# Kernel optimization log

Hardware: AMD Instinct MI355X
Metric: run time of the kernel (lower is better)

Reference implementation:

```python
import jax, jax.numpy as jnp
import numpy as np

V = 4          # number of views (fixed in module)
N = 1536       # number of regions/nodes
D = 256        # embedding_size
TOPK = 32      # top-k sparsification
NHEADS = 4     # MultiheadAttention heads
HD = D // NHEADS


def setup_inputs() -> dict:
    key = jax.random.key(0)
    ks = jax.random.split(key, 10)
    s = 1.0 / np.sqrt(D)
    return {
        "H": jax.random.normal(ks[0], (V, N, D), jnp.float32),
        "C": jax.random.uniform(ks[1], (V, V, N, N), jnp.float32),
        "WQ": jax.random.normal(ks[2], (V, D, D), jnp.float32) * s,
        "WK": jax.random.normal(ks[3], (V, D, D), jnp.float32) * s,
        "WV": jax.random.normal(ks[4], (V, D, D), jnp.float32) * s,
        "in_proj_w": jax.random.normal(ks[5], (3 * D, D), jnp.float32) * s,
        "in_proj_b": jnp.zeros((3 * D,), jnp.float32),
        "out_w": jax.random.normal(ks[6], (D, D), jnp.float32) * s,
        "out_b": jnp.zeros((D,), jnp.float32),
        "alphas": jnp.full((V,), 0.95, jnp.float32),   # [alpha_n, alpha_poi, alpha_s, alpha_d]
        "alpha_align": jnp.asarray(0.5, jnp.float32),
        "beta": jnp.asarray(0.5, jnp.float32),
    }


def reference(H, C, WQ, WK, WV, in_proj_w, in_proj_b, out_w, out_b, alphas, alpha_align, beta):
    # ---------------- IRCVA: MultiheadAttention over seq of 4 views, batch = N ----------------
    # H: (V, N, D); torch MHA (batch_first=False): L=V, batch=N
    qkv = jnp.einsum('lnd,ed->lne', H, in_proj_w) + in_proj_b       # (V, N, 3D)
    q, k, v = jnp.split(qkv, 3, axis=-1)

    def to_heads(x):  # (V, N, D) -> (N, h, V, hd)
        return x.reshape(V, N, NHEADS, HD).transpose(1, 2, 0, 3)

    qh, kh, vh = to_heads(q), to_heads(k), to_heads(v)
    att = jax.nn.softmax(jnp.einsum('nhld,nhmd->nhlm', qh, kh) / np.sqrt(HD), axis=-1)
    o = jnp.einsum('nhlm,nhmd->nhld', att, vh).transpose(2, 0, 1, 3).reshape(V, N, D)
    fusion = jnp.einsum('lnd,ed->lne', o, out_w) + out_b             # (V, N, D)
    a = alphas[:, None, None]
    aligned = fusion * a + (1.0 - a) * H                             # (V, N, D)

    # ---------------- CRCVA: top-k sparsified cross-view attention ----------------
    # per-view linear projections (torch Linear: y = x @ W.T)
    Qn = jnp.einsum('vnd,ved->vne', aligned, WQ)
    Kn = jnp.einsum('vnd,ved->vne', aligned, WK)
    Vn = jnp.einsum('vnd,ved->vne', aligned, WV)

    # row-wise top-k of C, scattered back to dense (V, V, N, N)
    vals, idx = jax.lax.top_k(C, TOPK)                               # (V, V, N, K)
    vi = jnp.arange(V)[:, None, None, None]
    qi = jnp.arange(V)[None, :, None, None]
    ni = jnp.arange(N)[None, None, :, None]
    sparse = jnp.zeros_like(C).at[vi, qi, ni, idx].set(vals)
    sparse = sparse * (1.0 - jnp.eye(V, dtype=C.dtype))[:, :, None, None]  # p==q pairs are zero
    C_hat = sparse / (jnp.sum(sparse, axis=-1, keepdims=True) + 1e-12)

    mask = (C_hat > 0).astype(C.dtype)
    scores = jnp.einsum('pnd,qmd->pqnm', Qn, Kn) / np.sqrt(D)        # (V, V, N, N)
    scores = scores * mask + (1.0 - mask) * (-1e9)
    alpha_nbr = jax.nn.softmax(scores, axis=-1)
    # original sums over ALL q (including q==p, which yields uniform attention -> mean of Vn[q])
    nbr = jnp.einsum('pqnm,qmd->pnd', alpha_nbr, Vn)                 # (V, N, D)

    # ---------------- fuse ----------------
    aa = jax.nn.sigmoid(alpha_align)
    f_fuse = jax.nn.relu(aa * aligned + (1.0 - aa) * nbr)
    b = jax.nn.sigmoid(beta)
    return b * H + (1.0 - b) * f_fuse                                # (V, N, D)
```

## Files before the change

kernel.cpp:

```cpp
#include <hip/hip_runtime.h>
#include <hip/hip_bf16.h>

#define VV 4
#define NN 1536
#define DD 256
#define TOPKN 32

typedef unsigned long long ull;
typedef unsigned int u32;
typedef unsigned short u16;
typedef __attribute__((ext_vector_type(8))) short bf16x8;
typedef __attribute__((ext_vector_type(4))) float f32x4;

__device__ __forceinline__ float us2f(u16 u) {
    return __uint_as_float(((u32)u) << 16);
}

__device__ __forceinline__ float sniff_scalar(const void* p, int idx) {
    const u16* u16p = (const u16*)p;
    float bf0 = us2f(u16p[0]);
    float a = fabsf(bf0);
    if (a > 0.01f && a < 100.0f) return us2f(u16p[idx]);
    return ((const float*)p)[idx];
}

__device__ __forceinline__ float gload(const void* p, size_t i, bool isbf) {
    return isbf ? us2f(((const u16*)p)[i]) : ((const float*)p)[i];
}

__device__ __forceinline__ void split_hl(float x, u16& h, u16& l) {
    u32 b = __float_as_uint(x);
    h = (u16)(b >> 16);
    float hf = __uint_as_float(b & 0xffff0000u);
    l = (u16)(__float_as_uint(x - hf) >> 16);
}

__device__ __forceinline__ int classify_wave(const void* p, int lane) {
    const u16* u = (const u16*)p;
    int z = 0, ins = 0;
    #pragma unroll
    for (int k0 = 0; k0 < 128; k0 += 64) {
        int k = k0 + lane;
        u16 lo = u[2 * k], hi = u[2 * k + 1];
        if (lo == 0) z++;
        if (((lo >> 7) & 0xFF) >= 133) ins++;
        if (((hi >> 7) & 0xFF) >= 133) ins++;
    }
    #pragma unroll
    for (int off = 32; off > 0; off >>= 1) {
        z += __shfl_xor(z, off, 64);
        ins += __shfl_xor(ins, off, 64);
    }
    if (z >= 100) return 0;
    if (ins >= 16) return 0;
    return 1;
}

__global__ __launch_bounds__(512) void sniff_kernel(
    const void* __restrict__ H, const void* __restrict__ C,
    const void* __restrict__ WQ, const void* __restrict__ WK,
    const void* __restrict__ WV, const void* __restrict__ inw,
    const void* __restrict__ outw, int* __restrict__ flags)
{
    int wv = threadIdx.x >> 6, lane = threadIdx.x & 63;
    const void* ps[7] = {H, C, WQ, WK, WV, inw, outw};
    if (wv < 7) {
        int f = classify_wave(ps[wv], lane);
        if (lane == 0) flags[wv] = f;
    }
}

__global__ __launch_bounds__(256) void prep_all(
    const void* __restrict__ H, const void* __restrict__ inw,
    const void* __restrict__ outw, const void* __restrict__ WQ,
    const void* __restrict__ WK, const void* __restrict__ WV,
    u16* __restrict__ Hh, u16* __restrict__ Hl,
    u16* __restrict__ iwh, u16* __restrict__ iwl,
    u16* __restrict__ owh, u16* __restrict__ owl,
    u16* __restrict__ wqh, u16* __restrict__ wql,
    u16* __restrict__ wkh, u16* __restrict__ wkl,
    u16* __restrict__ wvh, u16* __restrict__ wvl,
    const int* __restrict__ flags)
{
    const void* src; u16 *dh, *dl; int cnt, fi;
    switch (blockIdx.y) {
        case 0:  src = H;   dh = Hh;  dl = Hl;  cnt = 6144 * 256; fi = 0; break;
        case 1:  src = inw; dh = iwh; dl = iwl; cnt = 768 * 256;  fi = 5; break;
        case 2:  src = outw;dh = owh; dl = owl; cnt = 256 * 256;  fi = 6; break;
        case 3:  src = WQ;  dh = wqh; dl = wql; cnt = VV*256*256; fi = 2; break;
        case 4:  src = WK;  dh = wkh; dl = wkl; cnt = VV*256*256; fi = 3; break;
        default: src = WV;  dh = wvh; dl = wvl; cnt = VV*256*256; fi = 4; break;
    }
    int i0 = (blockIdx.x * 256 + threadIdx.x) * 4;
    if (i0 >= cnt) return;
    bool isbf = flags[fi] != 0;
    #pragma unroll
    for (int u = 0; u < 4; ++u) {
        float x = gload(src, (size_t)(i0 + u), isbf);
        u16 h, l;
        split_hl(x, h, l);
        dh[i0 + u] = h;
        dl[i0 + u] = l;
    }
}

template <int MODE>
__global__ __launch_bounds__(256) void gemm_mfma(
    const u16* __restrict__ Ah_, const u16* __restrict__ Al_,
    const u16* __restrict__ Bh_, const u16* __restrict__ Bl_,
    const u16* __restrict__ Bh2, const u16* __restrict__ Bl2,
    const u16* __restrict__ Bh3, const u16* __restrict__ Bl3,
    float* __restrict__ out0, float* __restrict__ out1, float* __restrict__ out2,
    u16* __restrict__ oH, u16* __restrict__ oL,
    int M, int E, int K,
    const void* __restrict__ Hin, const void* __restrict__ alphas,
    const int* __restrict__ flags)
{
    __shared__ __align__(16) u16 Ahs[128][40];
    __shared__ __align__(16) u16 Als[128][40];
    __shared__ __align__(16) u16 Bhs[128][40];
    __shared__ __align__(16) u16 Bls[128][40];

    int tid = threadIdx.x;
    int wv = tid >> 6, lane = tid & 63;
    int m0 = blockIdx.x * 128, e0 = blockIdx.y * 128;
    int wr = (wv >> 1) * 64, wc = (wv & 1) * 64;

    const u16* Ah = Ah_;
    const u16* Al = Al_;
    const u16* Bh = Bh_;
    const u16* Bl = Bl_;
    float* outp = out0;
    if (MODE == 2) {
        int v = blockIdx.z / 3, s = blockIdx.z % 3;
        size_t aOff = (size_t)v * (NN * 256);
        size_t bOff = (size_t)v * (256 * 256);
        Ah = Ah_ + aOff; Al = Al_ + aOff;
        Bh = (s == 0 ? Bh_ : s == 1 ? Bh2 : Bh3) + bOff;
        Bl = (s == 0 ? Bl_ : s == 1 ? Bl2 : Bl3) + bOff;
        outp = (s == 0 ? out0 : s == 1 ? out1 : out2) + (size_t)v * (NN * 256);
    }

    f32x4 acc[4][4];
    #pragma unroll
    for (int i = 0; i < 4; ++i)
        #pragma unroll
        for (int j = 0; j < 4; ++j)
            acc[i][j] = (f32x4){0.f, 0.f, 0.f, 0.f};

    int fr = lane & 15;
    int kg = (lane >> 4) << 3;

    for (int k0 = 0; k0 < K; k0 += 32) {
        #pragma unroll
        for (int q = 0; q < 2; ++q) {
            int idx8 = tid + (q << 8);
            int r = idx8 >> 2;
            int kc = (idx8 & 3) << 3;
            size_t ga = (size_t)(m0 + r) * K + k0 + kc;
            size_t gb = (size_t)(e0 + r) * K + k0 + kc;
            *(uint4*)&Ahs[r][kc] = *(const uint4*)(Ah + ga);
            *(uint4*)&Als[r][kc] = *(const uint4*)(Al + ga);
            *(uint4*)&Bhs[r][kc] = *(const uint4*)(Bh + gb);
            *(uint4*)&Bls[r][kc] = *(const uint4*)(Bl + gb);
        }
        __syncthreads();

        bf16x8 fah[4], fal[4], fbh[4], fbl[4];
        #pragma unroll
        for (int i = 0; i < 4; ++i) {
            fah[i] = *(const bf16x8*)&Ahs[wr + (i << 4) + fr][kg];
            fal[i] = *(const bf16x8*)&Als[wr + (i << 4) + fr][kg];
            fbh[i] = *(const bf16x8*)&Bhs[wc + (i << 4) + fr][kg];
            fbl[i] = *(const bf16x8*)&Bls[wc + (i << 4) + fr][kg];
        }
        #pragma unroll
        for (int i = 0; i < 4; ++i)
            #pragma unroll
            for (int j = 0; j < 4; ++j) {
                acc[i][j] = __builtin_amdgcn_mfma_f32_16x16x32_bf16(fah[i], fbh[j], acc[i][j], 0, 0, 0);
                acc[i][j] = __builtin_amdgcn_mfma_f32_16x16x32_bf16(fah[i], fbl[j], acc[i][j], 0, 0, 0);
                acc[i][j] = __builtin_amdgcn_mfma_f32_16x16x32_bf16(fal[i], fbh[j], acc[i][j], 0, 0, 0);
            }
        __syncthreads();
    }

    float a_epi = 0.f;
    bool h_bf = false;
    if (MODE == 1) {
        a_epi = sniff_scalar(alphas, m0 / NN);
        h_bf = flags[0] != 0;
    }
    int col = lane & 15;
    int rb = (lane >> 4) << 2;
    #pragma unroll
    for (int i = 0; i < 4; ++i)
        #pragma unroll
        for (int j = 0; j < 4; ++j)
            #pragma unroll
            for (int rr = 0; rr < 4; ++rr) {
                int m = m0 + wr + (i << 4) + rb + rr;
                int e = e0 + wc + (j << 4) + col;
                float v = acc[i][j][rr];
                size_t oi = (size_t)m * E + e;
                if (MODE == 1) {
                    float h = gload(Hin, oi, h_bf);
                    v = a_epi * v + (1.0f - a_epi) * h;
                    u16 hh, ll;
                    split_hl(v, hh, ll);
                    oH[oi] = hh;
                    oL[oi] = ll;
                }
                outp[oi] = v;
            }
}

__global__ __launch_bounds__(256) void attn_views(const float* __restrict__ qkv,
                                                  u16* __restrict__ oh,
                                                  u16* __restrict__ ol)
{
    int n = blockIdx.x;
    int t = threadIdx.x;
    __shared__ float qs[4][256], ks[4][256], vs[4][256];
    __shared__ float att[4][4][4];

    for (int l = 0; l < 4; ++l) {
        size_t base = ((size_t)l * NN + n) * 768;
        qs[l][t] = qkv[base + t];
        ks[l][t] = qkv[base + 256 + t];
        vs[l][t] = qkv[base + 512 + t];
    }
    __syncthreads();
    if (t < 64) {
        int h = t >> 4, l = (t >> 2) & 3, m = t & 3;
        float s = 0.f;
        #pragma unroll
        for (int d = 0; d < 64; ++d) s += qs[l][h * 64 + d] * ks[m][h * 64 + d];
        att[h][l][m] = s * 0.125f;
    }
    __syncthreads();
    if (t < 16) {
        int h = t >> 2, l = t & 3;
        float mx = -1e30f;
        for (int m = 0; m < 4; ++m) mx = fmaxf(mx, att[h][l][m]);
        float e[4], s = 0.f;
        for (int m = 0; m < 4; ++m) { e[m] = expf(att[h][l][m] - mx); s += e[m]; }
        for (int m = 0; m < 4; ++m) att[h][l][m] = e[m] / s;
    }
    __syncthreads();
    int h = t >> 6;
    for (int l = 0; l < 4; ++l) {
        float ov = 0.f;
        #pragma unroll
        for (int m = 0; m < 4; ++m) ov += att[h][l][m] * vs[m][t];
        u16 hh, ll;
        split_hl(ov, hh, ll);
        size_t oi = ((size_t)l * NN + n) * 256 + t;
        oh[oi] = hh;
        ol[oi] = ll;
    }
}

__global__ __launch_bounds__(256) void vbar_kernel(const float* __restrict__ Vn,
                                                   float* __restrict__ Vbar)
{
    int p = blockIdx.x >> 3, chunk = blockIdx.x & 7, d = threadIdx.x;
    const float* base = Vn + (size_t)p * NN * 256 + (size_t)chunk * 192 * 256 + d;
    float s = 0.f;
    for (int m = 0; m < 192; ++m) s += base[(size_t)m * 256];
    atomicAdd(&Vbar[p * 256 + d], s * (1.0f / 1536.0f));
}

#define TKTHR 0.9375f
#define TKCAP 192

__global__ __launch_bounds__(256) void topk_kernel(
    const void* __restrict__ Cp, const int* __restrict__ flags,
    int* __restrict__ tidx, float* __restrict__ tval)
{
    bool cbf = flags[1] != 0;
    int r = blockIdx.x;
    int p = r / (3 * NN);
    int rem = r % (3 * NN);
    int qi = rem / NN;
    int n = rem % NN;
    int q = qi + (qi >= p ? 1 : 0);
    size_t rowbase = (((size_t)p * VV + q) * NN + n) * (size_t)NN;

    int t = threadIdx.x;
    int lane = t & 63, wv = t >> 6;

    __shared__ ull cand[1536];
    __shared__ u32 cc;
    __shared__ int sel_idx[32];
    __shared__ u32 sel_key[32];

    if (t == 0) cc = 0;
    __syncthreads();

    if (!cbf) {
        const float4* row4 = (const float4*)((const float*)Cp + rowbase);
        for (int i = t; i < 384; i += 256) {
            float4 v = row4[i];
            int b = 4 * i;
            if (v.x > TKTHR) { u32 s = atomicAdd(&cc, 1u); if (s < TKCAP) cand[s] = (((ull)__float_as_uint(v.x)) << 16) | (ull)(2047 - b); }
            if (v.y > TKTHR) { u32 s = atomicAdd(&cc, 1u); if (s < TKCAP) cand[s] = (((ull)__float_as_uint(v.y)) << 16) | (ull)(2047 - (b + 1)); }
            if (v.z > TKTHR) { u32 s = atomicAdd(&cc, 1u); if (s < TKCAP) cand[s] = (((ull)__float_as_uint(v.z)) << 16) | (ull)(2047 - (b + 2)); }
            if (v.w > TKTHR) { u32 s = atomicAdd(&cc, 1u); if (s < TKCAP) cand[s] = (((ull)__float_as_uint(v.w)) << 16) | (ull)(2047 - (b + 3)); }
        }
    } else {
        for (int i = t; i < 1536; i += 256) {
            float v = us2f(((const u16*)Cp)[rowbase + i]);
            if (v > TKTHR) { u32 s = atomicAdd(&cc, 1u); if (s < TKCAP) cand[s] = (((ull)__float_as_uint(v)) << 16) | (ull)(2047 - i); }
        }
    }
    __syncthreads();
    int m = (int)cc;

    if (m >= TOPKN && m <= TKCAP) {
        if (t < m) {
            ull mykey = cand[t];
            int rank = 0;
            for (int c = 0; c < m; ++c) rank += (cand[c] > mykey) ? 1 : 0;
            if (rank < TOPKN) {
                sel_idx[rank] = 2047 - (int)(mykey & 0xFFFF);
                sel_key[rank] = (u32)(mykey >> 16);
            }
        }
    } else {
        if (!cbf) {
            const float4* row4 = (const float4*)((const float*)Cp + rowbase);
            for (int i = t; i < 384; i += 256) {
                float4 v = row4[i];
                int b = 4 * i;
                cand[b + 0] = (((ull)__float_as_uint(v.x)) << 16) | (ull)(2047 - b);
                cand[b + 1] = (((ull)__float_as_uint(v.y)) << 16) | (ull)(2047 - (b + 1));
                cand[b + 2] = (((ull)__float_as_uint(v.z)) << 16) | (ull)(2047 - (b + 2));
                cand[b + 3] = (((ull)__float_as_uint(v.w)) << 16) | (ull)(2047 - (b + 3));
            }
        } else {
            for (int i = t; i < 1536; i += 256) {
                float v = us2f(((const u16*)Cp)[rowbase + i]);
                cand[i] = (((ull)__float_as_uint(v)) << 16) | (ull)(2047 - i);
            }
        }
        __syncthreads();
        if (wv == 0) {
            for (int it = 0; it < TOPKN; ++it) {
                ull lm = 0;
                for (int c = lane; c < 1536; c += 64) { ull x = cand[c]; lm = x > lm ? x : lm; }
                #pragma unroll
                for (int off = 32; off > 0; off >>= 1) {
                    ull o2 = __shfl_xor(lm, off, 64);
                    lm = o2 > lm ? o2 : lm;
                }
                if (lane == 0) {
                    sel_idx[it] = 2047 - (int)(lm & 0xFFFF);
                    sel_key[it] = (u32)(lm >> 16);
                }
                for (int c = lane; c < 1536; c += 64) if (cand[c] == lm) cand[c] = 0;
            }
        }
    }
    __syncthreads();

    if (t < TOPKN) {
        tidx[(size_t)r * TOPKN + t] = sel_idx[t];
        tval[(size_t)r * TOPKN + t] = __uint_as_float(sel_key[t]);
    }
}

__global__ __launch_bounds__(256, 6) void nbr_final(
    const float* __restrict__ Qn, const float* __restrict__ Kn,
    const float* __restrict__ Vn, const float* __restrict__ Vbar,
    const float* __restrict__ alg, const void* __restrict__ Hin,
    const int* __restrict__ tidx, const float* __restrict__ tval,
    const void* __restrict__ a_align_p, const void* __restrict__ beta_p,
    const int* __restrict__ flags, float* __restrict__ out)
{
    bool h_bf = flags[0] != 0;
    int n = blockIdx.x, p = blockIdx.y, t = threadIdx.x;
    __shared__ __align__(16) float qv[256];
    __shared__ float sval[3][32];
    __shared__ float sbuf[3][32];
    __shared__ float att[3][32];
    __shared__ int sidx[3][32];

    size_t pn = (size_t)p * NN + n;
    qv[t] = Qn[pn * 256 + t];
    float acc = Vbar[p * 256 + t];
    if (t < 96) {
        int qi = t >> 5, j = t & 31;
        size_t r = ((size_t)(p * 3 + qi) * NN + n) * TOPKN;
        sidx[qi][j] = tidx[r + j];
        sval[qi][j] = tval[r + j];
    }
    __syncthreads();

    int j = t >> 3, prt = t & 7;
    #pragma unroll 1
    for (int qi = 0; qi < 3; ++qi) {
        int q = qi + (qi >= p ? 1 : 0);
        const float* krow = Kn + ((size_t)q * NN + sidx[qi][j]) * 256;
        float s = 0.f;
        #pragma unroll
        for (int i = 0; i < 8; ++i) {
            float4 kv = *(const float4*)(krow + (prt + 8 * i) * 4);
            float4 qq = *(const float4*)(&qv[(prt + 8 * i) * 4]);
            s = fmaf(kv.x, qq.x, fmaf(kv.y, qq.y, fmaf(kv.z, qq.z, fmaf(kv.w, qq.w, s))));
        }
        s += __shfl_xor(s, 1, 64);
        s += __shfl_xor(s, 2, 64);
        s += __shfl_xor(s, 4, 64);
        if (prt == 0) {
            float w = sval[qi][j];
            sbuf[qi][j] = (w > 0.f) ? s * 0.0625f : -1e30f;
        }
    }
    __syncthreads();

    if (t < 96) {
        int qi = t >> 5, jj = t & 31;
        float x = sbuf[qi][jj];
        float mx = x;
        #pragma unroll
        for (int off = 16; off > 0; off >>= 1)
            mx = fmaxf(mx, __shfl_xor(mx, off, 32));
        float e = expf(x - mx);
        float den = e;
        #pragma unroll
        for (int off = 16; off > 0; off >>= 1)
            den += __shfl_xor(den, off, 32);
        att[qi][jj] = (x > -1e29f) ? e / den : 0.f;
    }
    __syncthreads();

    #pragma unroll 1
    for (int qi = 0; qi < 3; ++qi) {
        int q = qi + (qi >= p ? 1 : 0);
        const float* vbase = Vn + (size_t)q * NN * 256 + t;
        #pragma unroll 1
        for (int j0 = 0; j0 < 32; j0 += 4) {
            float v0 = vbase[(size_t)sidx[qi][j0 + 0] * 256];
            float v1 = vbase[(size_t)sidx[qi][j0 + 1] * 256];
            float v2 = vbase[(size_t)sidx[qi][j0 + 2] * 256];
            float v3 = vbase[(size_t)sidx[qi][j0 + 3] * 256];
            acc = fmaf(att[qi][j0 + 0], v0, acc);
            acc = fmaf(att[qi][j0 + 1], v1, acc);
            acc = fmaf(att[qi][j0 + 2], v2, acc);
            acc = fmaf(att[qi][j0 + 3], v3, acc);
        }
    }

    float aa = 1.f / (1.f + expf(-sniff_scalar(a_align_p, 0)));
    float bb = 1.f / (1.f + expf(-sniff_scalar(beta_p, 0)));
    float al = alg[pn * 256 + t];
    float h = gload(Hin, pn * 256 + t, h_bf);
    float f = fmaxf(aa * al + (1.f - aa) * acc, 0.f);
    out[pn * 256 + t] = bb * h + (1.f - bb) * f;
}

extern "C" void kernel_launch(void* const* d_in, const int* in_sizes, int n_in,
                              void* d_out, int out_size, void* d_ws, size_t ws_size,
                              hipStream_t stream)
{
    const void* H       = d_in[0];
    const void* Cp      = d_in[1];
    const void* WQ      = d_in[2];
    const void* WK      = d_in[3];
    const void* WV      = d_in[4];
    const void* in_w    = d_in[5];
    const void* out_w   = d_in[7];
    const void* alphas  = d_in[9];
    const void* a_align = d_in[10];
    const void* beta    = d_in[11];
    float* out = (float*)d_out;

    float* ws   = (float*)d_ws;
    float* qkv  = ws;
    float* alg  = ws;
    float* Qn   = ws + 1572864;
    float* Kn   = ws + 3145728;
    float* tval = ws + 4718592;
    int*   tidx = (int*)(ws + 5308416);
    float* Vn   = ws + 6291456;
    float* Vbar = ws + 7864320;
    int*   flags = (int*)(ws + 7865344);

    u16* Hh   = (u16*)(ws + 7865360);
    u16* Hl   = (u16*)(ws + 8651792);
    u16* oh   = (u16*)(ws + 9438224);
    u16* ol   = (u16*)(ws + 10224656);
    u16* algh = (u16*)(ws + 11011088);
    u16* algl = (u16*)(ws + 11797520);
    u16* iwh  = (u16*)(ws + 12583952);
    u16* iwl  = (u16*)(ws + 12682256);
    u16* owh  = (u16*)(ws + 12780560);
    u16* owl  = (u16*)(ws + 12813328);
    u16* wqh  = (u16*)(ws + 12846096);
    u16* wql  = (u16*)(ws + 12977168);
    u16* wkh  = (u16*)(ws + 13108240);
    u16* wkl  = (u16*)(ws + 13239312);
    u16* wvh  = (u16*)(ws + 13370384);
    u16* wvl  = (u16*)(ws + 13501456);

    hipMemsetAsync(Vbar, 0, 1024 * sizeof(float), stream);

    sniff_kernel<<<1, 512, 0, stream>>>(H, Cp, WQ, WK, WV, in_w, out_w, flags);

    prep_all<<<dim3(1536, 6, 1), 256, 0, stream>>>(
        H, in_w, out_w, WQ, WK, WV,
        Hh, Hl, iwh, iwl, owh, owl, wqh, wql, wkh, wkl, wvh, wvl, flags);

    gemm_mfma<0><<<dim3(48, 6, 1), 256, 0, stream>>>(
        Hh, Hl, iwh, iwl, nullptr, nullptr, nullptr, nullptr,
        qkv, nullptr, nullptr, nullptr, nullptr,
        6144, 768, 256, nullptr, nullptr, flags);

    attn_views<<<NN, 256, 0, stream>>>(qkv, oh, ol);

    gemm_mfma<1><<<dim3(48, 2, 1), 256, 0, stream>>>(
        oh, ol, owh, owl, nullptr, nullptr, nullptr, nullptr,
        alg, nullptr, nullptr, algh, algl,
        6144, 256, 256, H, alphas, flags);

    gemm_mfma<2><<<dim3(12, 2, 12), 256, 0, stream>>>(
        algh, algl, wqh, wql, wkh, wkl, wvh, wvl,
        Qn, Kn, Vn, nullptr, nullptr,
        1536, 256, 256, nullptr, nullptr, flags);

    vbar_kernel<<<32, 256, 0, stream>>>(Vn, Vbar);
    topk_kernel<<<12 * NN, 256, 0, stream>>>(Cp, flags, tidx, tval);
    nbr_final<<<dim3(NN, VV), 256, 0, stream>>>(
        Qn, Kn, Vn, Vbar, alg, H, tidx, tval, a_align, beta, flags, out);
}
```

Measured before the change: 396.3 us.

## Fuse top-k row selection into the three GEMM launches as extra blocks

Removes the standalone top-k kernel and splits its 18432 rows into three chunks of 6144. Each chunk runs as extra blocks appended to one of the three MFMA GEMM launches, so the memory-bound C scan overlaps with the small, under-occupied GEMM grids. The GEMM tiles move to dynamic shared memory of 40 KB so both roles share one allocation, which may lower top-k occupancy compared with its old 12 KB footprint. The rank-counting loop is also vectorised to read candidates eight at a time from padded shared memory.

```diff
diff --git a/kernel.cpp b/kernel.cpp
--- a/kernel.cpp
+++ b/kernel.cpp
@@ -104,6 +104,117 @@
     }
 }
 
+#define TKTHR 0.9375f
+#define TKCAP 192
+
+__device__ void topk_body(const void* __restrict__ Cp,
+                          const int* __restrict__ flags,
+                          int* __restrict__ tidx, float* __restrict__ tval,
+                          int r, char* smem)
+{
+    bool cbf = flags[1] != 0;
+    int p = r / (3 * NN);
+    int rem = r % (3 * NN);
+    int qi = rem / NN;
+    int n = rem % NN;
+    int q = qi + (qi >= p ? 1 : 0);
+    size_t rowbase = (((size_t)p * VV + q) * NN + n) * (size_t)NN;
+
+    int t = threadIdx.x;
+    int lane = t & 63, wv = t >> 6;
+
+    ull* cand = (ull*)smem;
+    __shared__ u32 cc;
+    __shared__ int sel_idx[32];
+    __shared__ u32 sel_key[32];
+
+    if (t == 0) cc = 0;
+    __syncthreads();
+
+    if (!cbf) {
+        const float4* row4 = (const float4*)((const float*)Cp + rowbase);
+        for (int i = t; i < 384; i += 256) {
+            float4 v = row4[i];
+            int b = 4 * i;
+            if (v.x > TKTHR) { u32 s = atomicAdd(&cc, 1u); if (s < TKCAP) cand[s] = (((ull)__float_as_uint(v.x)) << 16) | (ull)(2047 - b); }
+            if (v.y > TKTHR) { u32 s = atomicAdd(&cc, 1u); if (s < TKCAP) cand[s] = (((ull)__float_as_uint(v.y)) << 16) | (ull)(2047 - (b + 1)); }
+            if (v.z > TKTHR) { u32 s = atomicAdd(&cc, 1u); if (s < TKCAP) cand[s] = (((ull)__float_as_uint(v.z)) << 16) | (ull)(2047 - (b + 2)); }
+            if (v.w > TKTHR) { u32 s = atomicAdd(&cc, 1u); if (s < TKCAP) cand[s] = (((ull)__float_as_uint(v.w)) << 16) | (ull)(2047 - (b + 3)); }
+        }
+    } else {
+        for (int i = t; i < 1536; i += 256) {
+            float v = us2f(((const u16*)Cp)[rowbase + i]);
+            if (v > TKTHR) { u32 s = atomicAdd(&cc, 1u); if (s < TKCAP) cand[s] = (((ull)__float_as_uint(v)) << 16) | (ull)(2047 - i); }
+        }
+    }
+    __syncthreads();
+    int m = (int)cc;
+
+    if (m >= TOPKN && m <= TKCAP) {
+        int mp = (m + 7) & ~7;
+        if (t < mp - m) cand[m + t] = 0;
+        __syncthreads();
+        if (t < m) {
+            ull mykey = cand[t];
+            int rank = 0;
+            for (int c = 0; c < mp; c += 8) {
+                ulonglong2 a0 = *(const ulonglong2*)&cand[c + 0];
+                ulonglong2 a1 = *(const ulonglong2*)&cand[c + 2];
+                ulonglong2 a2 = *(const ulonglong2*)&cand[c + 4];
+                ulonglong2 a3 = *(const ulonglong2*)&cand[c + 6];
+                rank += (a0.x > mykey) + (a0.y > mykey)
+                      + (a1.x > mykey) + (a1.y > mykey)
+                      + (a2.x > mykey) + (a2.y > mykey)
+                      + (a3.x > mykey) + (a3.y > mykey);
+            }
+            if (rank < TOPKN) {
+                sel_idx[rank] = 2047 - (int)(mykey & 0xFFFF);
+                sel_key[rank] = (u32)(mykey >> 16);
+            }
+        }
+    } else {
+        if (!cbf) {
+            const float4* row4 = (const float4*)((const float*)Cp + rowbase);
+            for (int i = t; i < 384; i += 256) {
+                float4 v = row4[i];
+                int b = 4 * i;
+                cand[b + 0] = (((ull)__float_as_uint(v.x)) << 16) | (ull)(2047 - b);
+                cand[b + 1] = (((ull)__float_as_uint(v.y)) << 16) | (ull)(2047 - (b + 1));
+                cand[b + 2] = (((ull)__float_as_uint(v.z)) << 16) | (ull)(2047 - (b + 2));
+                cand[b + 3] = (((ull)__float_as_uint(v.w)) << 16) | (ull)(2047 - (b + 3));
+            }
+        } else {
+            for (int i = t; i < 1536; i += 256) {
+                float v = us2f(((const u16*)Cp)[rowbase + i]);
+                cand[i] = (((ull)__float_as_uint(v)) << 16) | (ull)(2047 - i);
+            }
+        }
+        __syncthreads();
+        if (wv == 0) {
+            for (int it = 0; it < TOPKN; ++it) {
+                ull lm = 0;
+                for (int c = lane; c < 1536; c += 64) { ull x = cand[c]; lm = x > lm ? x : lm; }
+                #pragma unroll
+                for (int off = 32; off > 0; off >>= 1) {
+                    ull o2 = __shfl_xor(lm, off, 64);
+                    lm = o2 > lm ? o2 : lm;
+                }
+                if (lane == 0) {
+                    sel_idx[it] = 2047 - (int)(lm & 0xFFFF);
+                    sel_key[it] = (u32)(lm >> 16);
+                }
+                for (int c = lane; c < 1536; c += 64) if (cand[c] == lm) cand[c] = 0;
+            }
+        }
+    }
+    __syncthreads();
+
+    if (t < TOPKN) {
+        tidx[(size_t)r * TOPKN + t] = sel_idx[t];
+        tval[(size_t)r * TOPKN + t] = __uint_as_float(sel_key[t]);
+    }
+}
+
 template <int MODE>
 __global__ __launch_bounds__(256) void gemm_mfma(
     const u16* __restrict__ Ah_, const u16* __restrict__ Al_,
@@ -112,18 +223,31 @@
     const u16* __restrict__ Bh3, const u16* __restrict__ Bl3,
     float* __restrict__ out0, float* __restrict__ out1, float* __restrict__ out2,
     u16* __restrict__ oH, u16* __restrict__ oL,
-    int M, int E, int K,
+    int E, int K,
     const void* __restrict__ Hin, const void* __restrict__ alphas,
-    const int* __restrict__ flags)
-{
-    __shared__ __align__(16) u16 Ahs[128][40];
-    __shared__ __align__(16) u16 Als[128][40];
-    __shared__ __align__(16) u16 Bhs[128][40];
-    __shared__ __align__(16) u16 Bls[128][40];
+    const int* __restrict__ flags,
+    const void* __restrict__ Cp, int* __restrict__ tkidx, float* __restrict__ tkval,
+    int tk_base)
+{
+    extern __shared__ __align__(16) char smem[];
+    const int ngemm = (MODE == 1) ? 96 : 288;
+    int id = blockIdx.x;
+    if (id >= ngemm) {
+        topk_body(Cp, flags, tkidx, tkval, tk_base + id - ngemm, smem);
+        return;
+    }
+
+    u16* Ahs = (u16*)smem;
+    u16* Als = Ahs + 128 * 40;
+    u16* Bhs = Als + 128 * 40;
+    u16* Bls = Bhs + 128 * 40;
 
     int tid = threadIdx.x;
     int wv = tid >> 6, lane = tid & 63;
-    int m0 = blockIdx.x * 128, e0 = blockIdx.y * 128;
+    int bx, by, bz = 0;
+    if (MODE == 2) { bx = id % 12; by = (id / 12) % 2; bz = id / 24; }
+    else           { bx = id % 48; by = id / 48; }
+    int m0 = bx * 128, e0 = by * 128;
     int wr = (wv >> 1) * 64, wc = (wv & 1) * 64;
 
     const u16* Ah = Ah_;
@@ -132,7 +256,7 @@
     const u16* Bl = Bl_;
     float* outp = out0;
     if (MODE == 2) {
-        int v = blockIdx.z / 3, s = blockIdx.z % 3;
+        int v = bz / 3, s = bz % 3;
         size_t aOff = (size_t)v * (NN * 256);
         size_t bOff = (size_t)v * (256 * 256);
         Ah = Ah_ + aOff; Al = Al_ + aOff;
@@ -159,20 +283,20 @@
             int kc = (idx8 & 3) << 3;
             size_t ga = (size_t)(m0 + r) * K + k0 + kc;
             size_t gb = (size_t)(e0 + r) * K + k0 + kc;
-            *(uint4*)&Ahs[r][kc] = *(const uint4*)(Ah + ga);
-            *(uint4*)&Als[r][kc] = *(const uint4*)(Al + ga);
-            *(uint4*)&Bhs[r][kc] = *(const uint4*)(Bh + gb);
-            *(uint4*)&Bls[r][kc] = *(const uint4*)(Bl + gb);
+            *(uint4*)&Ahs[r * 40 + kc] = *(const uint4*)(Ah + ga);
+            *(uint4*)&Als[r * 40 + kc] = *(const uint4*)(Al + ga);
+            *(uint4*)&Bhs[r * 40 + kc] = *(const uint4*)(Bh + gb);
+            *(uint4*)&Bls[r * 40 + kc] = *(const uint4*)(Bl + gb);
         }
         __syncthreads();
 
         bf16x8 fah[4], fal[4], fbh[4], fbl[4];
         #pragma unroll
         for (int i = 0; i < 4; ++i) {
-            fah[i] = *(const bf16x8*)&Ahs[wr + (i << 4) + fr][kg];
-            fal[i] = *(const bf16x8*)&Als[wr + (i << 4) + fr][kg];
-            fbh[i] = *(const bf16x8*)&Bhs[wc + (i << 4) + fr][kg];
-            fbl[i] = *(const bf16x8*)&Bls[wc + (i << 4) + fr][kg];
+            fah[i] = *(const bf16x8*)&Ahs[(wr + (i << 4) + fr) * 40 + kg];
+            fal[i] = *(const bf16x8*)&Als[(wr + (i << 4) + fr) * 40 + kg];
+            fbh[i] = *(const bf16x8*)&Bhs[(wc + (i << 4) + fr) * 40 + kg];
+            fbl[i] = *(const bf16x8*)&Bls[(wc + (i << 4) + fr) * 40 + kg];
         }
         #pragma unroll
         for (int i = 0; i < 4; ++i)
@@ -271,105 +395,6 @@
     atomicAdd(&Vbar[p * 256 + d], s * (1.0f / 1536.0f));
 }
 
-#define TKTHR 0.9375f
-#define TKCAP 192
-
-__global__ __launch_bounds__(256) void topk_kernel(
-    const void* __restrict__ Cp, const int* __restrict__ flags,
-    int* __restrict__ tidx, float* __restrict__ tval)
-{
-    bool cbf = flags[1] != 0;
-    int r = blockIdx.x;
-    int p = r / (3 * NN);
-    int rem = r % (3 * NN);
-    int qi = rem / NN;
-    int n = rem % NN;
-    int q = qi + (qi >= p ? 1 : 0);
-    size_t rowbase = (((size_t)p * VV + q) * NN + n) * (size_t)NN;
-
-    int t = threadIdx.x;
-    int lane = t & 63, wv = t >> 6;
-
-    __shared__ ull cand[1536];
-    __shared__ u32 cc;
-    __shared__ int sel_idx[32];
-    __shared__ u32 sel_key[32];
-
-    if (t == 0) cc = 0;
-    __syncthreads();
-
-    if (!cbf) {
-        const float4* row4 = (const float4*)((const float*)Cp + rowbase);
-        for (int i = t; i < 384; i += 256) {
-            float4 v = row4[i];
-            int b = 4 * i;
-            if (v.x > TKTHR) { u32 s = atomicAdd(&cc, 1u); if (s < TKCAP) cand[s] = (((ull)__float_as_uint(v.x)) << 16) | (ull)(2047 - b); }
-            if (v.y > TKTHR) { u32 s = atomicAdd(&cc, 1u); if (s < TKCAP) cand[s] = (((ull)__float_as_uint(v.y)) << 16) | (ull)(2047 - (b + 1)); }
-            if (v.z > TKTHR) { u32 s = atomicAdd(&cc, 1u); if (s < TKCAP) cand[s] = (((ull)__float_as_uint(v.z)) << 16) | (ull)(2047 - (b + 2)); }
-            if (v.w > TKTHR) { u32 s = atomicAdd(&cc, 1u); if (s < TKCAP) cand[s] = (((ull)__float_as_uint(v.w)) << 16) | (ull)(2047 - (b + 3)); }
-        }
-    } else {
-        for (int i = t; i < 1536; i += 256) {
-            float v = us2f(((const u16*)Cp)[rowbase + i]);
-            if (v > TKTHR) { u32 s = atomicAdd(&cc, 1u); if (s < TKCAP) cand[s] = (((ull)__float_as_uint(v)) << 16) | (ull)(2047 - i); }
-        }
-    }
-    __syncthreads();
-    int m = (int)cc;
-
-    if (m >= TOPKN && m <= TKCAP) {
-        if (t < m) {
-            ull mykey = cand[t];
-            int rank = 0;
-            for (int c = 0; c < m; ++c) rank += (cand[c] > mykey) ? 1 : 0;
-            if (rank < TOPKN) {
-                sel_idx[rank] = 2047 - (int)(mykey & 0xFFFF);
-                sel_key[rank] = (u32)(mykey >> 16);
-            }
-        }
-    } else {
-        if (!cbf) {
-            const float4* row4 = (const float4*)((const float*)Cp + rowbase);
-            for (int i = t; i < 384; i += 256) {
-                float4 v = row4[i];
-                int b = 4 * i;
-                cand[b + 0] = (((ull)__float_as_uint(v.x)) << 16) | (ull)(2047 - b);
-                cand[b + 1] = (((ull)__float_as_uint(v.y)) << 16) | (ull)(2047 - (b + 1));
-                cand[b + 2] = (((ull)__float_as_uint(v.z)) << 16) | (ull)(2047 - (b + 2));
-                cand[b + 3] = (((ull)__float_as_uint(v.w)) << 16) | (ull)(2047 - (b + 3));
-            }
-        } else {
-            for (int i = t; i < 1536; i += 256) {
-                float v = us2f(((const u16*)Cp)[rowbase + i]);
-                cand[i] = (((ull)__float_as_uint(v)) << 16) | (ull)(2047 - i);
-            }
-        }
-        __syncthreads();
-        if (wv == 0) {
-            for (int it = 0; it < TOPKN; ++it) {
-                ull lm = 0;
-                for (int c = lane; c < 1536; c += 64) { ull x = cand[c]; lm = x > lm ? x : lm; }
-                #pragma unroll
-                for (int off = 32; off > 0; off >>= 1) {
-                    ull o2 = __shfl_xor(lm, off, 64);
-                    lm = o2 > lm ? o2 : lm;
-                }
-                if (lane == 0) {
-                    sel_idx[it] = 2047 - (int)(lm & 0xFFFF);
-                    sel_key[it] = (u32)(lm >> 16);
-                }
-                for (int c = lane; c < 1536; c += 64) if (cand[c] == lm) cand[c] = 0;
-            }
-        }
-    }
-    __syncthreads();
-
-    if (t < TOPKN) {
-        tidx[(size_t)r * TOPKN + t] = sel_idx[t];
-        tval[(size_t)r * TOPKN + t] = __uint_as_float(sel_key[t]);
-    }
-}
-
 __global__ __launch_bounds__(256, 6) void nbr_final(
     const float* __restrict__ Qn, const float* __restrict__ Kn,
     const float* __restrict__ Vn, const float* __restrict__ Vbar,
@@ -504,6 +529,8 @@
     u16* wvh  = (u16*)(ws + 13370384);
     u16* wvl  = (u16*)(ws + 13501456);
 
+    const int SMEM = 40960;
+
     hipMemsetAsync(Vbar, 0, 1024 * sizeof(float), stream);
 
     sniff_kernel<<<1, 512, 0, stream>>>(H, Cp, WQ, WK, WV, in_w, out_w, flags);
@@ -512,25 +539,27 @@
         H, in_w, out_w, WQ, WK, WV,
         Hh, Hl, iwh, iwl, owh, owl, wqh, wql, wkh, wkl, wvh, wvl, flags);
 
-    gemm_mfma<0><<<dim3(48, 6, 1), 256, 0, stream>>>(
+    gemm_mfma<0><<<288 + 6144, 256, SMEM, stream>>>(
         Hh, Hl, iwh, iwl, nullptr, nullptr, nullptr, nullptr,
         qkv, nullptr, nullptr, nullptr, nullptr,
-        6144, 768, 256, nullptr, nullptr, flags);
+        768, 256, nullptr, nullptr, flags,
+        Cp, tidx, tval, 0);
 
     attn_views<<<NN, 256, 0, stream>>>(qkv, oh, ol);
 
-    gemm_mfma<1><<<dim3(48, 2, 1), 256, 0, stream>>>(
+    gemm_mfma<1><<<96 + 6144, 256, SMEM, stream>>>(
         oh, ol, owh, owl, nullptr, nullptr, nullptr, nullptr,
         alg, nullptr, nullptr, algh, algl,
-        6144, 256, 256, H, alphas, flags);
-
-    gemm_mfma<2><<<dim3(12, 2, 12), 256, 0, stream>>>(
+        256, 256, H, alphas, flags,
+        Cp, tidx, tval, 6144);
+
+    gemm_mfma<2><<<288 + 6144, 256, SMEM, stream>>>(
         algh, algl, wqh, wql, wkh, wkl, wvh, wvl,
         Qn, Kn, Vn, nullptr, nullptr,
-        1536, 256, 256, nullptr, nullptr, flags);
+        256, 256, nullptr, nullptr, flags,
+        Cp, tidx, tval, 12288);
 
     vbar_kernel<<<32, 256, 0, stream>>>(Vn, Vbar);
-    topk_kernel<<<12 * NN, 256, 0, stream>>>(Cp, flags, tidx, tval);
     nbr_final<<<dim3(NN, VV), 256, 0, stream>>>(
         Qn, Kn, Vn, Vbar, alg, H, tidx, tval, a_align, beta, flags, out);
 }
```

New measurement: 508.9 us. 1.28x slower.

## Split top-k into global-atomic filter pass and separate selection kernel

Applied to the files above, without the earlier changes.

Breaks the top-k kernel into a filter kernel, which streams each C row and appends above-threshold candidates to a global buffer using global atomics, and a select kernel, which ranks those candidates with vectorized LDS reads. The fallback path now rereads C from global memory in each iteration instead of holding the full row in shared memory. Launching the filter right after the sniff step moves it ahead of the GEMMs, and the select kernel uses little shared memory so more blocks can be resident. The costs are an extra memset, a global candidate buffer round trip, and global atomic contention, all in exchange for lighter and more parallel kernels.

```diff
diff --git a/kernel.cpp b/kernel.cpp
--- a/kernel.cpp
+++ b/kernel.cpp
@@ -274,9 +274,13 @@
 #define TKTHR 0.9375f
 #define TKCAP 192
 
-__global__ __launch_bounds__(256) void topk_kernel(
+__device__ __forceinline__ ull tk_pack(float v, int i) {
+    return (((ull)__float_as_uint(v)) << 16) | (ull)(2047 - i);
+}
+
+__global__ __launch_bounds__(256) void topk_filter(
     const void* __restrict__ Cp, const int* __restrict__ flags,
-    int* __restrict__ tidx, float* __restrict__ tval)
+    ull* __restrict__ candbuf, u32* __restrict__ cnt)
 {
     bool cbf = flags[1] != 0;
     int r = blockIdx.x;
@@ -286,80 +290,101 @@
     int n = rem % NN;
     int q = qi + (qi >= p ? 1 : 0);
     size_t rowbase = (((size_t)p * VV + q) * NN + n) * (size_t)NN;
-
     int t = threadIdx.x;
-    int lane = t & 63, wv = t >> 6;
-
-    __shared__ ull cand[1536];
-    __shared__ u32 cc;
+    ull* cb = candbuf + (size_t)r * TKCAP;
+
+    if (!cbf) {
+        const float4* row4 = (const float4*)((const float*)Cp + rowbase);
+        float4 v0 = row4[t];
+        int b0 = 4 * t;
+        if (v0.x > TKTHR) { u32 s = atomicAdd(&cnt[r], 1u); if (s < TKCAP) cb[s] = tk_pack(v0.x, b0 + 0); }
+        if (v0.y > TKTHR) { u32 s = atomicAdd(&cnt[r], 1u); if (s < TKCAP) cb[s] = tk_pack(v0.y, b0 + 1); }
+        if (v0.z > TKTHR) { u32 s = atomicAdd(&cnt[r], 1u); if (s < TKCAP) cb[s] = tk_pack(v0.z, b0 + 2); }
+        if (v0.w > TKTHR) { u32 s = atomicAdd(&cnt[r], 1u); if (s < TKCAP) cb[s] = tk_pack(v0.w, b0 + 3); }
+        if (t < 128) {
+            float4 v1 = row4[256 + t];
+            int b1 = 4 * (256 + t);
+            if (v1.x > TKTHR) { u32 s = atomicAdd(&cnt[r], 1u); if (s < TKCAP) cb[s] = tk_pack(v1.x, b1 + 0); }
+            if (v1.y > TKTHR) { u32 s = atomicAdd(&cnt[r], 1u); if (s < TKCAP) cb[s] = tk_pack(v1.y, b1 + 1); }
+            if (v1.z > TKTHR) { u32 s = atomicAdd(&cnt[r], 1u); if (s < TKCAP) cb[s] = tk_pack(v1.z, b1 + 2); }
+            if (v1.w > TKTHR) { u32 s = atomicAdd(&cnt[r], 1u); if (s < TKCAP) cb[s] = tk_pack(v1.w, b1 + 3); }
+        }
+    } else {
+        #pragma unroll
+        for (int u = 0; u < 6; ++u) {
+            int i = t + 256 * u;
+            float v = us2f(((const u16*)Cp)[rowbase + i]);
+            if (v > TKTHR) { u32 s = atomicAdd(&cnt[r], 1u); if (s < TKCAP) cb[s] = tk_pack(v, i); }
+        }
+    }
+}
+
+__global__ __launch_bounds__(192) void topk_select(
+    const void* __restrict__ Cp, const int* __restrict__ flags,
+    const ull* __restrict__ candbuf, const u32* __restrict__ cnt,
+    int* __restrict__ tidx, float* __restrict__ tval)
+{
+    int r = blockIdx.x;
+    int t = threadIdx.x;
+    __shared__ __align__(16) ull cl[TKCAP];
     __shared__ int sel_idx[32];
     __shared__ u32 sel_key[32];
-
-    if (t == 0) cc = 0;
-    __syncthreads();
-
-    if (!cbf) {
-        const float4* row4 = (const float4*)((const float*)Cp + rowbase);
-        for (int i = t; i < 384; i += 256) {
-            float4 v = row4[i];
-            int b = 4 * i;
-            if (v.x > TKTHR) { u32 s = atomicAdd(&cc, 1u); if (s < TKCAP) cand[s] = (((ull)__float_as_uint(v.x)) << 16) | (ull)(2047 - b); }
-            if (v.y > TKTHR) { u32 s = atomicAdd(&cc, 1u); if (s < TKCAP) cand[s] = (((ull)__float_as_uint(v.y)) << 16) | (ull)(2047 - (b + 1)); }
-            if (v.z > TKTHR) { u32 s = atomicAdd(&cc, 1u); if (s < TKCAP) cand[s] = (((ull)__float_as_uint(v.z)) << 16) | (ull)(2047 - (b + 2)); }
-            if (v.w > TKTHR) { u32 s = atomicAdd(&cc, 1u); if (s < TKCAP) cand[s] = (((ull)__float_as_uint(v.w)) << 16) | (ull)(2047 - (b + 3)); }
-        }
-    } else {
-        for (int i = t; i < 1536; i += 256) {
-            float v = us2f(((const u16*)Cp)[rowbase + i]);
-            if (v > TKTHR) { u32 s = atomicAdd(&cc, 1u); if (s < TKCAP) cand[s] = (((ull)__float_as_uint(v)) << 16) | (ull)(2047 - i); }
-        }
-    }
-    __syncthreads();
-    int m = (int)cc;
+    __shared__ ull red[192];
+
+    int m = (int)cnt[r];
+    const ull* cb = candbuf + (size_t)r * TKCAP;
 
     if (m >= TOPKN && m <= TKCAP) {
+        int mp = (m + 7) & ~7;
+        if (t < m) cl[t] = cb[t];
+        else if (t < mp) cl[t] = 0;
+        __syncthreads();
         if (t < m) {
-            ull mykey = cand[t];
+            ull mykey = cl[t];
             int rank = 0;
-            for (int c = 0; c < m; ++c) rank += (cand[c] > mykey) ? 1 : 0;
+            for (int c = 0; c < mp; c += 8) {
+                ulonglong2 a0 = *(const ulonglong2*)&cl[c + 0];
+                ulonglong2 a1 = *(const ulonglong2*)&cl[c + 2];
+                ulonglong2 a2 = *(const ulonglong2*)&cl[c + 4];
+                ulonglong2 a3 = *(const ulonglong2*)&cl[c + 6];
+                rank += (a0.x > mykey) + (a0.y > mykey)
+                      + (a1.x > mykey) + (a1.y > mykey)
+                      + (a2.x > mykey) + (a2.y > mykey)
+                      + (a3.x > mykey) + (a3.y > mykey);
+            }
             if (rank < TOPKN) {
                 sel_idx[rank] = 2047 - (int)(mykey & 0xFFFF);
                 sel_key[rank] = (u32)(mykey >> 16);
             }
         }
     } else {
-        if (!cbf) {
-            const float4* row4 = (const float4*)((const float*)Cp + rowbase);
-            for (int i = t; i < 384; i += 256) {
-                float4 v = row4[i];
-                int b = 4 * i;
-                cand[b + 0] = (((ull)__float_as_uint(v.x)) << 16) | (ull)(2047 - b);
-                cand[b + 1] = (((ull)__float_as_uint(v.y)) << 16) | (ull)(2047 - (b + 1));
-                cand[b + 2] = (((ull)__float_as_uint(v.z)) << 16) | (ull)(2047 - (b + 2));
-                cand[b + 3] = (((ull)__float_as_uint(v.w)) << 16) | (ull)(2047 - (b + 3));
+        bool cbf = flags[1] != 0;
+        int p = r / (3 * NN);
+        int rem = r % (3 * NN);
+        int qi = rem / NN;
+        int n = rem % NN;
+        int q = qi + (qi >= p ? 1 : 0);
+        size_t rowbase = (((size_t)p * VV + q) * NN + n) * (size_t)NN;
+        for (int it = 0; it < TOPKN; ++it) {
+            ull lm = 0;
+            for (int i = t; i < 1536; i += 192) {
+                bool skip = false;
+                for (int s2 = 0; s2 < it; ++s2) if (sel_idx[s2] == i) skip = true;
+                if (!skip) {
+                    float v = gload(Cp, rowbase + i, cbf);
+                    ull key = tk_pack(v, i);
+                    if (key > lm) lm = key;
+                }
             }
-        } else {
-            for (int i = t; i < 1536; i += 256) {
-                float v = us2f(((const u16*)Cp)[rowbase + i]);
-                cand[i] = (((ull)__float_as_uint(v)) << 16) | (ull)(2047 - i);
+            red[t] = lm;
+            __syncthreads();
+            if (t == 0) {
+                ull best = 0;
+                for (int x = 0; x < 192; ++x) if (red[x] > best) best = red[x];
+                sel_idx[it] = 2047 - (int)(best & 0xFFFF);
+                sel_key[it] = (u32)(best >> 16);
             }
-        }
-        __syncthreads();
-        if (wv == 0) {
-            for (int it = 0; it < TOPKN; ++it) {
-                ull lm = 0;
-                for (int c = lane; c < 1536; c += 64) { ull x = cand[c]; lm = x > lm ? x : lm; }
-                #pragma unroll
-                for (int off = 32; off > 0; off >>= 1) {
-                    ull o2 = __shfl_xor(lm, off, 64);
-                    lm = o2 > lm ? o2 : lm;
-                }
-                if (lane == 0) {
-                    sel_idx[it] = 2047 - (int)(lm & 0xFFFF);
-                    sel_key[it] = (u32)(lm >> 16);
-                }
-                for (int c = lane; c < 1536; c += 64) if (cand[c] == lm) cand[c] = 0;
-            }
+            __syncthreads();
         }
     }
     __syncthreads();
@@ -504,9 +529,15 @@
     u16* wvh  = (u16*)(ws + 13370384);
     u16* wvl  = (u16*)(ws + 13501456);
 
+    u32* tkcnt   = (u32*)(ws + 13632528);
+    ull* candbuf = (ull*)(ws + 13650960);
+
     hipMemsetAsync(Vbar, 0, 1024 * sizeof(float), stream);
+    hipMemsetAsync(tkcnt, 0, 18432 * sizeof(u32), stream);
 
     sniff_kernel<<<1, 512, 0, stream>>>(H, Cp, WQ, WK, WV, in_w, out_w, flags);
+
+    topk_filter<<<18432, 256, 0, stream>>>(Cp, flags, candbuf, tkcnt);
 
     prep_all<<<dim3(1536, 6, 1), 256, 0, stream>>>(
         H, in_w, out_w, WQ, WK, WV,
@@ -530,7 +561,9 @@
         1536, 256, 256, nullptr, nullptr, flags);
 
     vbar_kernel<<<32, 256, 0, stream>>>(Vn, Vbar);
-    topk_kernel<<<12 * NN, 256, 0, stream>>>(Cp, flags, tidx, tval);
+
+    topk_select<<<18432, 192, 0, stream>>>(Cp, flags, candbuf, tkcnt, tidx, tval);
+
     nbr_final<<<dim3(NN, VV), 256, 0, stream>>>(
         Qn, Kn, Vn, Vbar, alg, H, tidx, tval, a_align, beta, flags, out);
 }
```

Result: slower. 455.3 us (+14.9%).
